# Kernel optimization log

Hardware: AMD Instinct MI355X
Metric: run time of the kernel (lower is better)

## Reference

```python
import jax, jax.numpy as jnp
import numpy as np

H = 768        # hidden_size == embedding_dim (forced by GRU input 3*H)
S = 512        # seq_len
V = 30522      # vocab_size
MAXLEN = 32    # decode steps
B = 8
NEG = -1e6


def setup_inputs() -> dict:
    key = jax.random.key(0)
    ks = jax.random.split(key, 12)
    sd = 0.02
    return {
        "encoder_outputs": jax.random.normal(ks[0], (B, S, H), jnp.float32),
        "inputs": jax.random.randint(ks[1], (B, S), 0, V),
        "cls_to": 101,
        "sep_to": 102,
        "emb": jax.random.normal(ks[2], (V, H), jnp.float32) * sd,
        "attn_w": jax.random.normal(ks[3], (H, H), jnp.float32) * sd,
        "attn_b": jnp.zeros((H,), jnp.float32),
        "copy_w": jax.random.normal(ks[4], (H, H), jnp.float32) * sd,
        "copy_b": jnp.zeros((H,), jnp.float32),
        "gru_w_ih": jax.random.normal(ks[5], (3 * H, 3 * H), jnp.float32) * sd,
        "gru_w_hh": jax.random.normal(ks[6], (3 * H, H), jnp.float32) * sd,
        "gru_b_ih": jnp.zeros((3 * H,), jnp.float32),
        "gru_b_hh": jnp.zeros((3 * H,), jnp.float32),
        "out_w": jax.random.normal(ks[7], (V, H), jnp.float32) * sd,
        "out_b": jnp.zeros((V,), jnp.float32),
    }


def _gru_cell(x, h, w_ih, w_hh, b_ih, b_hh):
    # PyTorch GRU cell, gate order (r, z, n)
    gi = x @ w_ih.T + b_ih          # [B, 3H]
    gh = h @ w_hh.T + b_hh          # [B, 3H]
    gi_r, gi_z, gi_n = jnp.split(gi, 3, axis=-1)
    gh_r, gh_z, gh_n = jnp.split(gh, 3, axis=-1)
    r = jax.nn.sigmoid(gi_r + gh_r)
    z = jax.nn.sigmoid(gi_z + gh_z)
    n = jnp.tanh(gi_n + r * gh_n)
    return (1.0 - z) * n + z * h


def reference(encoder_outputs, inputs, cls_to, sep_to, emb, attn_w, attn_b,
              copy_w, copy_b, gru_w_ih, gru_w_hh, gru_b_ih, gru_b_hh,
              out_w, out_b):
    dtype = encoder_outputs.dtype
    ext = V + S  # extended vocab (vocab + seq positions)
    one_hot = jax.nn.one_hot(inputs, ext, dtype=dtype)          # [B, S, V+S]
    missing = (one_hot.sum(axis=1) == 0).at[:, 0].set(True)     # [B, V+S]

    def step(carry, _):
        hidden, idx, sel = carry  # [B,H], [B] int, [B,H]
        # attention
        th = hidden @ attn_w.T + attn_b                          # [B,H]
        attn_scores = jnp.einsum('bsh,bh->bs', encoder_outputs, th)
        attn_weights = jax.nn.softmax(attn_scores, axis=-1)
        context = jnp.einsum('bs,bsh->bh', attn_weights, encoder_outputs)
        # embed previous token (OOV -> UNK id 3; note original uses strict >)
        idx_c = jnp.where(idx > V, 3, idx)
        embedded = emb[idx_c]                                    # [B,H]
        # GRU step
        x = jnp.concatenate([context, sel, embedded], axis=-1)   # [B,3H]
        h = _gru_cell(x, hidden, gru_w_ih, gru_w_hh, gru_b_ih, gru_b_hh)
        # copy scores
        th2 = h @ copy_w.T + copy_b
        copy_score_seq = jnp.einsum('bsh,bh->bs', encoder_outputs, th2)  # [B,S]
        copy_scores = jnp.einsum('bs,bsv->bv', copy_score_seq, one_hot)  # [B,V+S]
        copy_scores = jnp.where(missing, NEG, copy_scores)
        # generation scores
        gen = (h @ out_w.T + out_b).at[:, 0].set(NEG)            # [B,V]
        combined = jnp.concatenate([gen, copy_scores], axis=-1)  # [B,2V+S]
        probs = jax.nn.softmax(combined, axis=-1)
        gen_probs = jnp.concatenate(
            [probs[:, :V], jnp.zeros((B, S), dtype)], axis=-1)   # [B,V+S]
        final_probs = gen_probs + probs[:, V:]
        log_probs = jnp.log(final_probs + 1e-10)                 # [B,V+S]
        sampled = jnp.argmax(log_probs, axis=-1)                 # [B]
        # selective read for next step
        pos = jnp.take_along_axis(one_hot, sampled[:, None, None], axis=2)[..., 0]  # [B,S]
        sel_scores = pos * copy_score_seq
        denom = jnp.maximum(jnp.sum(jnp.abs(sel_scores), axis=1, keepdims=True), 1e-12)
        sel_new = jnp.einsum('bs,bsh->bh', sel_scores / denom, encoder_outputs)
        return (h, sampled, sel_new), (log_probs, sampled)

    init = (jnp.zeros((B, H), dtype),
            jnp.ones((B,), jnp.int32),
            jnp.zeros((B, H), dtype))
    _, (logps, samples) = jax.lax.scan(step, init, None, length=MAXLEN - 1)

    sos = jnp.zeros((B, ext), dtype).at[:, 0].set(cls_to)
    decoder_outputs = jnp.concatenate(
        [sos[:, None, :], jnp.swapaxes(logps, 0, 1)], axis=1)    # [B,MAXLEN,V+S]
    sampled_idxs = jnp.concatenate(
        [jnp.ones((B, 1), samples.dtype), samples.T], axis=1)    # [B,MAXLEN]
    return decoder_outputs, sampled_idxs
```

## Files before the change

kernel.cpp:

```cpp
#include <hip/hip_runtime.h>
#include <hip/hip_bf16.h>
#include <math.h>

#define HDIM 768
#define SDIM 512
#define VDIM 30522
#define BDIM 8
#define TLEN 32
#define H3   2304
#define VT   31034
#define NEGV -1.0e6f
#define OFF2 ((size_t)BDIM * TLEN * VT)
#define SSLICE 64
#define VSLICE 3816
#define NROWS (HDIM + VDIM + HDIM + H3)

__global__ __launch_bounds__(256) void boot_kernel(
    float* __restrict__ dout, const int* __restrict__ cls,
    float* __restrict__ hA, float* __restrict__ x,
    const float* __restrict__ emb, float* __restrict__ thb,
    float* __restrict__ ghb, const float* __restrict__ attn_b,
    const float* __restrict__ b_hh)
{
    int gidx = blockIdx.x * 256 + threadIdx.x;
    int stride = gridDim.x * 256;
    float clsv = (float)cls[0];
    for (int i = gidx; i < BDIM * VT; i += stride) {
        int b = i / VT, v = i % VT;
        dout[(size_t)b * TLEN * VT + v] = (v == 0) ? clsv : 0.f;
    }
    if (gidx < BDIM) dout[OFF2 + (size_t)gidx * TLEN] = 1.0f;
    for (int i = gidx; i < BDIM * HDIM; i += stride) {
        int b = i / HDIM, j = i % HDIM;
        hA[i] = 0.f;
        x[b * H3 + HDIM + j] = 0.f;
        x[b * H3 + 2 * HDIM + j] = emb[HDIM + j];
        thb[i] = attn_b[j];
    }
    for (int i = gidx; i < BDIM * H3; i += stride)
        ghb[i] = b_hh[i % H3];
}

__global__ __launch_bounds__(512) void grufull_kernel(
    const float* __restrict__ w_ih, const float* __restrict__ b_ih,
    const float* __restrict__ x, const float* __restrict__ ghb,
    const float* __restrict__ hin, float* __restrict__ hout)
{
    int wid = threadIdx.x >> 6, lane = threadIdx.x & 63;
    int j = blockIdx.x * 8 + wid;
    if (j >= HDIM) return;

    const float4* wr = (const float4*)(w_ih + (size_t)j * H3);
    const float4* wz = (const float4*)(w_ih + (size_t)(HDIM + j) * H3);
    const float4* wn = (const float4*)(w_ih + (size_t)(2 * HDIM + j) * H3);

    float ar[8], az[8], an[8];
#pragma unroll
    for (int b = 0; b < 8; b++) { ar[b] = 0.f; az[b] = 0.f; an[b] = 0.f; }

    for (int k4 = lane; k4 < H3 / 4; k4 += 64) {
        float4 w4r = wr[k4], w4z = wz[k4], w4n = wn[k4];
#pragma unroll
        for (int b = 0; b < 8; b++) {
            float4 x4 = ((const float4*)(x + b * H3))[k4];
            ar[b] += w4r.x * x4.x + w4r.y * x4.y + w4r.z * x4.z + w4r.w * x4.w;
            az[b] += w4z.x * x4.x + w4z.y * x4.y + w4z.z * x4.z + w4z.w * x4.w;
            an[b] += w4n.x * x4.x + w4n.y * x4.y + w4n.z * x4.z + w4n.w * x4.w;
        }
    }
#pragma unroll
    for (int b = 0; b < 8; b++) {
        float vr = ar[b], vz = az[b], vn = an[b];
        for (int off = 32; off; off >>= 1) {
            vr += __shfl_down(vr, off, 64);
            vz += __shfl_down(vz, off, 64);
            vn += __shfl_down(vn, off, 64);
        }
        ar[b] = vr; az[b] = vz; an[b] = vn;
    }
    if (lane == 0) {
        float bi_r = b_ih[j], bi_z = b_ih[HDIM + j], bi_n = b_ih[2 * HDIM + j];
#pragma unroll
        for (int b = 0; b < 8; b++) {
            float gir = ar[b] + bi_r;
            float giz = az[b] + bi_z;
            float gin = an[b] + bi_n;
            float ghr = ghb[b * H3 + j];
            float ghz = ghb[b * H3 + HDIM + j];
            float ghn = ghb[b * H3 + 2 * HDIM + j];
            float r = 1.f / (1.f + expf(-(gir + ghr)));
            float z = 1.f / (1.f + expf(-(giz + ghz)));
            float n = tanhf(gin + r * ghn);
            hout[b * HDIM + j] = (1.f - z) * n + z * hin[b * HDIM + j];
        }
    }
}

struct RowT { const float* w; const float* bias; float* dst; int stride; int neg; };

__device__ __forceinline__ RowT row_info(
    int r,
    const float* copy_w, const float* copy_b,
    const float* out_w,  const float* out_b,
    const float* attn_w, const float* attn_b,
    const float* w_hh,   const float* b_hh,
    float* th2, float* gen, float* thb, float* ghb)
{
    RowT t;
    if (r < HDIM) {
        t.w = copy_w + (size_t)r * HDIM; t.bias = copy_b + r;
        t.dst = th2 + r; t.stride = HDIM; t.neg = 0;
    } else if (r < HDIM + VDIM) {
        int v = r - HDIM;
        t.w = out_w + (size_t)v * HDIM; t.bias = out_b + v;
        t.dst = gen + v; t.stride = VDIM; t.neg = (v == 0);
    } else if (r < 2 * HDIM + VDIM) {
        int rr = r - HDIM - VDIM;
        t.w = attn_w + (size_t)rr * HDIM; t.bias = attn_b + rr;
        t.dst = thb + rr; t.stride = HDIM; t.neg = 0;
    } else {
        int rr = r - 2 * HDIM - VDIM;
        t.w = w_hh + (size_t)rr * HDIM; t.bias = b_hh + rr;
        t.dst = ghb + rr; t.stride = H3; t.neg = 0;
    }
    return t;
}

__global__ __launch_bounds__(256) void bigmv_kernel(
    const float* __restrict__ copy_w, const float* __restrict__ copy_b,
    const float* __restrict__ out_w,  const float* __restrict__ out_b,
    const float* __restrict__ attn_w, const float* __restrict__ attn_b,
    const float* __restrict__ w_hh,   const float* __restrict__ b_hh,
    const float* __restrict__ hp, float* __restrict__ th2,
    float* __restrict__ gen, float* __restrict__ thb,
    float* __restrict__ ghb)
{
    __shared__ float xs[BDIM * HDIM];
    {
        const float4* s4 = (const float4*)hp;
        float4* d4 = (float4*)xs;
#pragma unroll
        for (int i = 0; i < 6; i++)
            d4[threadIdx.x + i * 256] = s4[threadIdx.x + i * 256];
    }
    __syncthreads();

    int wid = threadIdx.x >> 6, lane = threadIdx.x & 63;
    int r0 = blockIdx.x * 16 + wid * 4;
    if (r0 >= NROWS) return;

    int rc1 = min(r0 + 1, NROWS - 1);
    int rc2 = min(r0 + 2, NROWS - 1), rc3 = min(r0 + 3, NROWS - 1);
    RowT t0 = row_info(r0,  copy_w, copy_b, out_w, out_b, attn_w, attn_b,
                       w_hh, b_hh, th2, gen, thb, ghb);
    RowT t1 = row_info(rc1, copy_w, copy_b, out_w, out_b, attn_w, attn_b,
                       w_hh, b_hh, th2, gen, thb, ghb);
    RowT t2 = row_info(rc2, copy_w, copy_b, out_w, out_b, attn_w, attn_b,
                       w_hh, b_hh, th2, gen, thb, ghb);
    RowT t3 = row_info(rc3, copy_w, copy_b, out_w, out_b, attn_w, attn_b,
                       w_hh, b_hh, th2, gen, thb, ghb);

    float a0[8], a1[8], a2[8], a3[8];
#pragma unroll
    for (int b = 0; b < 8; b++) { a0[b] = 0.f; a1[b] = 0.f; a2[b] = 0.f; a3[b] = 0.f; }

    const float4* w0 = (const float4*)t0.w;
    const float4* w1 = (const float4*)t1.w;
    const float4* w2 = (const float4*)t2.w;
    const float4* w3 = (const float4*)t3.w;

#pragma unroll
    for (int i = 0; i < 3; i++) {
        int k4 = lane + i * 64;
        float4 q0 = w0[k4], q1 = w1[k4], q2 = w2[k4], q3 = w3[k4];
#pragma unroll
        for (int b = 0; b < 8; b++) {
            float4 x4 = ((const float4*)(xs + b * HDIM))[k4];
            a0[b] += q0.x * x4.x + q0.y * x4.y + q0.z * x4.z + q0.w * x4.w;
            a1[b] += q1.x * x4.x + q1.y * x4.y + q1.z * x4.z + q1.w * x4.w;
            a2[b] += q2.x * x4.x + q2.y * x4.y + q2.z * x4.z + q2.w * x4.w;
            a3[b] += q3.x * x4.x + q3.y * x4.y + q3.z * x4.z + q3.w * x4.w;
        }
    }
#pragma unroll
    for (int b = 0; b < 8; b++) {
        float v0 = a0[b], v1 = a1[b], v2 = a2[b], v3 = a3[b];
        for (int off = 32; off; off >>= 1) {
            v0 += __shfl_down(v0, off, 64);
            v1 += __shfl_down(v1, off, 64);
            v2 += __shfl_down(v2, off, 64);
            v3 += __shfl_down(v3, off, 64);
        }
        a0[b] = v0; a1[b] = v1; a2[b] = v2; a3[b] = v3;
    }
    if (lane == 0) {
        float bb0 = t0.bias[0], bb1 = t1.bias[0], bb2 = t2.bias[0], bb3 = t3.bias[0];
#pragma unroll
        for (int b = 0; b < 8; b++) {
            t0.dst[(size_t)b * t0.stride] = t0.neg ? NEGV : a0[b] + bb0;
            if (r0 + 1 < NROWS) t1.dst[(size_t)b * t1.stride] = t1.neg ? NEGV : a1[b] + bb1;
            if (r0 + 2 < NROWS) t2.dst[(size_t)b * t2.stride] = t2.neg ? NEGV : a2[b] + bb2;
            if (r0 + 3 < NROWS) t3.dst[(size_t)b * t3.stride] = t3.neg ? NEGV : a3[b] + bb3;
        }
    }
}

__global__ __launch_bounds__(512) void combo_kernel(
    const float* __restrict__ enc, const float* __restrict__ thb,
    const float* __restrict__ th2, float* __restrict__ css,
    float* __restrict__ atC, float* __restrict__ atM, float* __restrict__ atZ,
    const float* __restrict__ gen, float* __restrict__ gM,
    float* __restrict__ gZ, int do_cg)
{
    __shared__ float sth[HDIM];
    __shared__ float sth2[HDIM];
    __shared__ float swe[SSLICE];
    __shared__ float red[8];
    int blk = blockIdx.x, b = blk >> 3, sub = blk & 7;
    int tid = threadIdx.x, wid = tid >> 6, lane = tid & 63;
    int slo = sub * SSLICE;

    for (int i = tid; i < HDIM; i += 512) {
        sth[i]  = thb[b * HDIM + i];
        sth2[i] = th2[b * HDIM + i];
    }
    __syncthreads();

    for (int j = 0; j < 8; j++) {
        int sl = wid * 8 + j, s = slo + sl;
        const float4* er = (const float4*)(enc + ((size_t)b * SDIM + s) * HDIM);
        float a1 = 0.f, a2 = 0.f;
#pragma unroll
        for (int i = 0; i < 3; i++) {
            float4 e = er[lane + i * 64];
            float4 t1 = ((const float4*)sth)[lane + i * 64];
            float4 t2 = ((const float4*)sth2)[lane + i * 64];
            a1 += e.x * t1.x + e.y * t1.y + e.z * t1.z + e.w * t1.w;
            a2 += e.x * t2.x + e.y * t2.y + e.z * t2.z + e.w * t2.w;
        }
        for (int off = 32; off; off >>= 1) {
            a1 += __shfl_down(a1, off, 64);
            a2 += __shfl_down(a2, off, 64);
        }
        if (lane == 0) {
            swe[sl] = a1;
            if (do_cg) css[b * SDIM + s] = a2;
        }
    }
    __syncthreads();

    if (tid < 64) {
        float v = swe[tid];
        float m = v;
        for (int off = 32; off; off >>= 1) m = fmaxf(m, __shfl_xor(m, off, 64));
        float e = expf(v - m);
        float z = e;
        for (int off = 32; off; off >>= 1) z += __shfl_xor(z, off, 64);
        swe[tid] = e;
        if (tid == 0) { atM[b * 8 + sub] = m; atZ[b * 8 + sub] = z; }
    }
    __syncthreads();

    for (int col = tid; col < HDIM; col += 512) {
        float acc = 0.f;
        const float* eb = enc + ((size_t)b * SDIM + slo) * HDIM + col;
#pragma unroll 8
        for (int s2 = 0; s2 < SSLICE; s2++) acc += swe[s2] * eb[s2 * HDIM];
        atC[((size_t)b * 8 + sub) * HDIM + col] = acc;
    }

    if (!do_cg) return;

    int vlo = sub * VSLICE, vhi = min(VDIM, vlo + VSLICE);
    const float* grow = gen + (size_t)b * VDIM;
    float m = -INFINITY;
    for (int v = vlo + tid; v < vhi; v += 512) m = fmaxf(m, grow[v]);
    for (int off = 32; off; off >>= 1) m = fmaxf(m, __shfl_xor(m, off, 64));
    if (lane == 0) red[wid] = m;
    __syncthreads();
    float M = red[0];
#pragma unroll
    for (int w = 1; w < 8; w++) M = fmaxf(M, red[w]);
    float z = 0.f;
    for (int v = vlo + tid; v < vhi; v += 512) z += expf(grow[v] - M);
    for (int off = 32; off; off >>= 1) z += __shfl_xor(z, off, 64);
    __syncthreads();
    if (lane == 0) red[wid] = z;
    __syncthreads();
    if (tid == 0) {
        float Z = 0.f;
#pragma unroll
        for (int w = 0; w < 8; w++) Z += red[w];
        gM[b * 8 + sub] = M;
        gZ[b * 8 + sub] = Z;
    }
}

__global__ __launch_bounds__(1024) void tailc_kernel(
    const float* __restrict__ gen, const float* __restrict__ css,
    const int* __restrict__ inputs, const float* __restrict__ genM,
    const float* __restrict__ genZ, float* __restrict__ dout,
    float* __restrict__ argV, int* __restrict__ argI, int t)
{
    __shared__ int   toks[SDIM];
    __shared__ float csss[SDIM];
    __shared__ float aggv[SDIM];
    __shared__ unsigned char ffl[SDIM];
    __shared__ float redf[1024];
    __shared__ int   redi[1024];
    int blk = blockIdx.x, b = blk >> 3, sub = blk & 7;
    int tid = threadIdx.x;

    if (tid < SDIM) {
        toks[tid] = inputs[b * SDIM + tid];
        csss[tid] = css[b * SDIM + tid];
    }
    __syncthreads();

    if (tid < SDIM) {
        int tok = toks[tid]; int isf = 0; float agg = -INFINITY;
        if (tok != 0) {
            isf = 1;
            for (int s2 = 0; s2 < tid; s2++)
                if (toks[s2] == tok) { isf = 0; break; }
            if (isf) {
                float ss = 0.f;
                for (int s2 = tid; s2 < SDIM; s2++)
                    if (toks[s2] == tok) ss += csss[s2];
                agg = ss;
            }
        }
        ffl[tid] = (unsigned char)isf;
        aggv[tid] = agg;
    }
    __syncthreads();

    redf[tid] = (tid < SDIM && ffl[tid]) ? aggv[tid] : -INFINITY;
    __syncthreads();
    for (int off = 512; off; off >>= 1) {
        if (tid < off) redf[tid] = fmaxf(redf[tid], redf[tid + off]);
        __syncthreads();
    }
    float m9 = redf[0]; __syncthreads();
    redf[tid] = (tid < SDIM && ffl[tid] && m9 > -INFINITY)
                    ? expf(aggv[tid] - m9) : 0.f;
    __syncthreads();
    for (int off = 512; off; off >>= 1) {
        if (tid < off) redf[tid] += redf[tid + off];
        __syncthreads();
    }
    float z9 = redf[0]; __syncthreads();

    float M = genM[b * 8 + 0];
#pragma unroll
    for (int i = 1; i < 8; i++) M = fmaxf(M, genM[b * 8 + i]);
    if (m9 > -INFINITY) M = fmaxf(M, m9);
    float Z = 0.f;
#pragma unroll
    for (int i = 0; i < 8; i++) Z += genZ[b * 8 + i] * expf(genM[b * 8 + i] - M);
    if (m9 > -INFINITY) Z += z9 * expf(m9 - M);
    float invZ = 1.f / Z;

    const float* grow = gen + (size_t)b * VDIM;
    float* orow = dout + ((size_t)b * TLEN + t + 1) * VT;
    int vlo = sub * VSLICE, vhi = min(VDIM, vlo + VSLICE);
    float best = -INFINITY; int bidx = 2147483647;
    for (int v = vlo + tid; v < vhi; v += 1024) {
        float pg = expf(grow[v] - M) * invZ;
        float lp = logf(pg + 1e-10f);
        orow[v] = lp;
        if (lp > best) { best = lp; bidx = v; }
    }
    if (sub == 0 && tid < SDIM) orow[VDIM + tid] = logf(1e-10f);
    __syncthreads();

    if (tid < SDIM && ffl[tid]) {
        int tok = toks[tid];
        if (tok >= vlo && tok < vhi) {
            float pc = expf(aggv[tid] - M) * invZ;
            float pg = expf(grow[tok] - M) * invZ;
            float lp = logf(pg + pc + 1e-10f);
            orow[tok] = lp;
            if (lp > best || (lp == best && tok < bidx)) { best = lp; bidx = tok; }
        }
    }
    redf[tid] = best; redi[tid] = bidx; __syncthreads();
    for (int off = 512; off; off >>= 1) {
        if (tid < off) {
            float v2 = redf[tid + off]; int i2 = redi[tid + off];
            if (v2 > redf[tid] || (v2 == redf[tid] && i2 < redi[tid])) {
                redf[tid] = v2; redi[tid] = i2;
            }
        }
        __syncthreads();
    }
    if (tid == 0) { argV[b * 8 + sub] = redf[0]; argI[b * 8 + sub] = redi[0]; }
}

__global__ __launch_bounds__(1024) void mix_kernel(
    const float* __restrict__ enc, const float* __restrict__ css,
    const int* __restrict__ inputs, const float* __restrict__ argV,
    const int* __restrict__ argI, const float* __restrict__ emb,
    float* __restrict__ dout, float* __restrict__ x,
    const float* __restrict__ atC, const float* __restrict__ atM,
    const float* __restrict__ atZ, int t, int do_tail)
{
    __shared__ int   toks[SDIM];
    __shared__ float csss[SDIM];
    __shared__ float redf[1024];
    __shared__ int   mlist[SDIM];
    __shared__ float mscore[SDIM];
    __shared__ int   wcnt[16], woff[16];
    __shared__ int   mtot;
    int bid = blockIdx.x, tid = threadIdx.x;

    if (bid >= BDIM) {
        int b = bid - BDIM;
        if (tid < HDIM) {
            float m[8], z[8];
#pragma unroll
            for (int i = 0; i < 8; i++) { m[i] = atM[b * 8 + i]; z[i] = atZ[b * 8 + i]; }
            float M = m[0];
#pragma unroll
            for (int i = 1; i < 8; i++) M = fmaxf(M, m[i]);
            float Z = 0.f;
#pragma unroll
            for (int i = 0; i < 8; i++) Z += z[i] * expf(m[i] - M);
            float acc = 0.f;
#pragma unroll
            for (int i = 0; i < 8; i++)
                acc += atC[((size_t)b * 8 + i) * HDIM + tid] * expf(m[i] - M);
            x[b * H3 + tid] = acc / Z;
        }
        return;
    }
    if (!do_tail) return;

    int b = bid;
    float best = argV[b * 8 + 0]; int samp = argI[b * 8 + 0];
#pragma unroll
    for (int i = 1; i < 8; i++) {
        float v = argV[b * 8 + i];
        if (v > best) { best = v; samp = argI[b * 8 + i]; }
    }
    if (tid == 0) dout[OFF2 + (size_t)b * TLEN + t + 1] = (float)samp;

    if (tid < SDIM) {
        toks[tid] = inputs[b * SDIM + tid];
        csss[tid] = css[b * SDIM + tid];
    }
    __syncthreads();

    int flag = (tid < SDIM) ? (toks[tid] == samp) : 0;
    redf[tid] = flag ? fabsf(csss[tid]) : 0.f;
    __syncthreads();
    for (int off = 512; off; off >>= 1) {
        if (tid < off) redf[tid] += redf[tid + off];
        __syncthreads();
    }
    float den = fmaxf(redf[0], 1e-12f);
    __syncthreads();

    unsigned long long mk = __ballot(flag);
    int wv = tid >> 6, ln = tid & 63;
    if (ln == 0) wcnt[wv] = __popcll(mk);
    __syncthreads();
    if (tid == 0) {
        int o = 0;
        for (int w = 0; w < 16; w++) { woff[w] = o; o += wcnt[w]; }
        mtot = o;
    }
    __syncthreads();
    if (flag) {
        int pos = woff[wv] + __popcll(mk & ((1ULL << ln) - 1ULL));
        mlist[pos] = tid;
        mscore[pos] = csss[tid] / den;
    }
    __syncthreads();
    int mc = mtot;

    if (tid < HDIM) {
        float sel = 0.f;
        for (int mI = 0; mI < mc; mI++)
            sel += mscore[mI] * enc[((size_t)b * SDIM + mlist[mI]) * HDIM + tid];
        x[b * H3 + HDIM + tid] = sel;
        int ic = (samp > VDIM) ? 3 : samp;
        if (ic >= VDIM) ic = VDIM - 1;
        x[b * H3 + 2 * HDIM + tid] = emb[(size_t)ic * HDIM + tid];
    }
}

extern "C" void kernel_launch(void* const* d_in, const int* in_sizes, int n_in,
                              void* d_out, int out_size, void* d_ws, size_t ws_size,
                              hipStream_t stream)
{
    const float* enc    = (const float*)d_in[0];
    const int*   inputs = (const int*)d_in[1];
    const int*   cls    = (const int*)d_in[2];
    const float* emb    = (const float*)d_in[4];
    const float* attn_w = (const float*)d_in[5];
    const float* attn_b = (const float*)d_in[6];
    const float* copy_w = (const float*)d_in[7];
    const float* copy_b = (const float*)d_in[8];
    const float* w_ih   = (const float*)d_in[9];
    const float* w_hh   = (const float*)d_in[10];
    const float* b_ih   = (const float*)d_in[11];
    const float* b_hh   = (const float*)d_in[12];
    const float* out_w  = (const float*)d_in[13];
    const float* out_b  = (const float*)d_in[14];
    float* dout = (float*)d_out;

    float* ws   = (float*)d_ws;
    float* hA   = ws;
    float* hB   = hA  + BDIM * HDIM;
    float* x    = hB  + BDIM * HDIM;
    float* thb  = x   + BDIM * H3;
    float* ghb  = thb + BDIM * HDIM;
    float* th2  = ghb + BDIM * H3;
    float* gen  = th2 + BDIM * HDIM;
    float* css  = gen + (size_t)BDIM * VDIM;
    float* atC  = css + BDIM * SDIM;
    float* atM  = atC + BDIM * 8 * HDIM;
    float* atZ  = atM + 64;
    float* gM   = atZ + 64;
    float* gZ   = gM  + 64;
    float* argV = gZ  + 64;
    int*   argI = (int*)(argV + 64);

    boot_kernel<<<512, 256, 0, stream>>>(dout, cls, hA, x, emb, thb, ghb,
                                         attn_b, b_hh);
    combo_kernel<<<64, 512, 0, stream>>>(enc, thb, th2, css, atC, atM, atZ,
                                         gen, gM, gZ, 0);
    mix_kernel<<<16, 1024, 0, stream>>>(enc, css, inputs, argV, argI, emb,
                                        dout, x, atC, atM, atZ, 0, 0);

    for (int t = 0; t < TLEN - 1; t++) {
        const float* hin  = (t & 1) ? hB : hA;
        float*       hout = (t & 1) ? hA : hB;
        grufull_kernel<<<96, 512, 0, stream>>>(w_ih, b_ih, x, ghb, hin, hout);
        bigmv_kernel<<<(NROWS + 15) / 16, 256, 0, stream>>>(
            copy_w, copy_b, out_w, out_b, attn_w, attn_b, w_hh, b_hh,
            hout, th2, gen, thb, ghb);
        combo_kernel<<<64, 512, 0, stream>>>(enc, thb, th2, css, atC, atM, atZ,
                                             gen, gM, gZ, 1);
        tailc_kernel<<<64, 1024, 0, stream>>>(gen, css, inputs, gM, gZ,
                                              dout, argV, argI, t);
        mix_kernel<<<16, 1024, 0, stream>>>(enc, css, inputs, argV, argI, emb,
                                            dout, x, atC, atM, atZ, t, 1);
    }
}
```

Measured before the change: 3.342 ms.

## Split attention and vocab slices finer and use one-wave GRU blocks

The combo kernel's sequence and vocab split goes from 8 to 32 sub-slices per batch row, so it launches 256 blocks instead of 64. The mix and tail kernels now merge 32 partial softmax results instead of 8. The GRU kernel moves to one 64-thread block per hidden unit for more independent blocks. The bigmv kernel drops its shared-memory staging of the hidden state and reads it straight from global memory, relying on cache. The aim is better GPU occupancy on the latency-bound per-step kernels, at the cost of more partial-merge work and more repeated global reads of the hidden state.

New measurement: 3.298 ms. About the same (-1.3%).

```diff
diff --git a/kernel.cpp b/kernel.cpp
--- a/kernel.cpp
+++ b/kernel.cpp
@@ -11,7 +11,9 @@
 #define VT   31034
 #define NEGV -1.0e6f
 #define OFF2 ((size_t)BDIM * TLEN * VT)
-#define SSLICE 64
+#define NSUB 32
+#define SSL  16
+#define VSL  954
 #define VSLICE 3816
 #define NROWS (HDIM + VDIM + HDIM + H3)
 
@@ -41,14 +43,13 @@
         ghb[i] = b_hh[i % H3];
 }
 
-__global__ __launch_bounds__(512) void grufull_kernel(
+__global__ __launch_bounds__(64) void grufull_kernel(
     const float* __restrict__ w_ih, const float* __restrict__ b_ih,
     const float* __restrict__ x, const float* __restrict__ ghb,
     const float* __restrict__ hin, float* __restrict__ hout)
 {
-    int wid = threadIdx.x >> 6, lane = threadIdx.x & 63;
-    int j = blockIdx.x * 8 + wid;
-    if (j >= HDIM) return;
+    int lane = threadIdx.x;
+    int j = blockIdx.x;
 
     const float4* wr = (const float4*)(w_ih + (size_t)j * H3);
     const float4* wz = (const float4*)(w_ih + (size_t)(HDIM + j) * H3);
@@ -135,16 +136,6 @@
     float* __restrict__ gen, float* __restrict__ thb,
     float* __restrict__ ghb)
 {
-    __shared__ float xs[BDIM * HDIM];
-    {
-        const float4* s4 = (const float4*)hp;
-        float4* d4 = (float4*)xs;
-#pragma unroll
-        for (int i = 0; i < 6; i++)
-            d4[threadIdx.x + i * 256] = s4[threadIdx.x + i * 256];
-    }
-    __syncthreads();
-
     int wid = threadIdx.x >> 6, lane = threadIdx.x & 63;
     int r0 = blockIdx.x * 16 + wid * 4;
     if (r0 >= NROWS) return;
@@ -168,6 +159,7 @@
     const float4* w1 = (const float4*)t1.w;
     const float4* w2 = (const float4*)t2.w;
     const float4* w3 = (const float4*)t3.w;
+    const float4* xb = (const float4*)hp;
 
 #pragma unroll
     for (int i = 0; i < 3; i++) {
@@ -175,7 +167,7 @@
         float4 q0 = w0[k4], q1 = w1[k4], q2 = w2[k4], q3 = w3[k4];
 #pragma unroll
         for (int b = 0; b < 8; b++) {
-            float4 x4 = ((const float4*)(xs + b * HDIM))[k4];
+            float4 x4 = xb[b * 192 + k4];
             a0[b] += q0.x * x4.x + q0.y * x4.y + q0.z * x4.z + q0.w * x4.w;
             a1[b] += q1.x * x4.x + q1.y * x4.y + q1.z * x4.z + q1.w * x4.w;
             a2[b] += q2.x * x4.x + q2.y * x4.y + q2.z * x4.z + q2.w * x4.w;
@@ -214,11 +206,11 @@
 {
     __shared__ float sth[HDIM];
     __shared__ float sth2[HDIM];
-    __shared__ float swe[SSLICE];
+    __shared__ float swe[SSL];
     __shared__ float red[8];
-    int blk = blockIdx.x, b = blk >> 3, sub = blk & 7;
+    int blk = blockIdx.x, b = blk >> 5, sub = blk & 31;
     int tid = threadIdx.x, wid = tid >> 6, lane = tid & 63;
-    int slo = sub * SSLICE;
+    int slo = sub * SSL;
 
     for (int i = tid; i < HDIM; i += 512) {
         sth[i]  = thb[b * HDIM + i];
@@ -226,8 +218,8 @@
     }
     __syncthreads();
 
-    for (int j = 0; j < 8; j++) {
-        int sl = wid * 8 + j, s = slo + sl;
+    for (int j = 0; j < 2; j++) {
+        int sl = wid * 2 + j, s = slo + sl;
         const float4* er = (const float4*)(enc + ((size_t)b * SDIM + s) * HDIM);
         float a1 = 0.f, a2 = 0.f;
 #pragma unroll
@@ -249,29 +241,27 @@
     }
     __syncthreads();
 
-    if (tid < 64) {
-        float v = swe[tid];
-        float m = v;
-        for (int off = 32; off; off >>= 1) m = fmaxf(m, __shfl_xor(m, off, 64));
-        float e = expf(v - m);
-        float z = e;
-        for (int off = 32; off; off >>= 1) z += __shfl_xor(z, off, 64);
-        swe[tid] = e;
-        if (tid == 0) { atM[b * 8 + sub] = m; atZ[b * 8 + sub] = z; }
+    if (tid == 0) {
+        float m = swe[0];
+        for (int i = 1; i < SSL; i++) m = fmaxf(m, swe[i]);
+        float z = 0.f;
+        for (int i = 0; i < SSL; i++) { float e = expf(swe[i] - m); swe[i] = e; z += e; }
+        atM[b * NSUB + sub] = m;
+        atZ[b * NSUB + sub] = z;
     }
     __syncthreads();
 
     for (int col = tid; col < HDIM; col += 512) {
         float acc = 0.f;
         const float* eb = enc + ((size_t)b * SDIM + slo) * HDIM + col;
-#pragma unroll 8
-        for (int s2 = 0; s2 < SSLICE; s2++) acc += swe[s2] * eb[s2 * HDIM];
-        atC[((size_t)b * 8 + sub) * HDIM + col] = acc;
+#pragma unroll
+        for (int s2 = 0; s2 < SSL; s2++) acc += swe[s2] * eb[s2 * HDIM];
+        atC[((size_t)b * NSUB + sub) * HDIM + col] = acc;
     }
 
     if (!do_cg) return;
 
-    int vlo = sub * VSLICE, vhi = min(VDIM, vlo + VSLICE);
+    int vlo = sub * VSL, vhi = min(VDIM, vlo + VSL);
     const float* grow = gen + (size_t)b * VDIM;
     float m = -INFINITY;
     for (int v = vlo + tid; v < vhi; v += 512) m = fmaxf(m, grow[v]);
@@ -291,8 +281,8 @@
         float Z = 0.f;
 #pragma unroll
         for (int w = 0; w < 8; w++) Z += red[w];
-        gM[b * 8 + sub] = M;
-        gZ[b * 8 + sub] = Z;
+        gM[b * NSUB + sub] = M;
+        gZ[b * NSUB + sub] = Z;
     }
 }
 
@@ -351,13 +341,14 @@
     }
     float z9 = redf[0]; __syncthreads();
 
-    float M = genM[b * 8 + 0];
-#pragma unroll
-    for (int i = 1; i < 8; i++) M = fmaxf(M, genM[b * 8 + i]);
+    float M = genM[b * NSUB + 0];
+#pragma unroll
+    for (int i = 1; i < NSUB; i++) M = fmaxf(M, genM[b * NSUB + i]);
     if (m9 > -INFINITY) M = fmaxf(M, m9);
     float Z = 0.f;
 #pragma unroll
-    for (int i = 0; i < 8; i++) Z += genZ[b * 8 + i] * expf(genM[b * 8 + i] - M);
+    for (int i = 0; i < NSUB; i++)
+        Z += genZ[b * NSUB + i] * expf(genM[b * NSUB + i] - M);
     if (m9 > -INFINITY) Z += z9 * expf(m9 - M);
     float invZ = 1.f / Z;
 
@@ -417,19 +408,16 @@
     if (bid >= BDIM) {
         int b = bid - BDIM;
         if (tid < HDIM) {
-            float m[8], z[8];
-#pragma unroll
-            for (int i = 0; i < 8; i++) { m[i] = atM[b * 8 + i]; z[i] = atZ[b * 8 + i]; }
-            float M = m[0];
-#pragma unroll
-            for (int i = 1; i < 8; i++) M = fmaxf(M, m[i]);
-            float Z = 0.f;
-#pragma unroll
-            for (int i = 0; i < 8; i++) Z += z[i] * expf(m[i] - M);
-            float acc = 0.f;
-#pragma unroll
-            for (int i = 0; i < 8; i++)
-                acc += atC[((size_t)b * 8 + i) * HDIM + tid] * expf(m[i] - M);
+            float M = atM[b * NSUB];
+#pragma unroll
+            for (int i = 1; i < NSUB; i++) M = fmaxf(M, atM[b * NSUB + i]);
+            float Z = 0.f, acc = 0.f;
+#pragma unroll
+            for (int i = 0; i < NSUB; i++) {
+                float sc = expf(atM[b * NSUB + i] - M);
+                Z += atZ[b * NSUB + i] * sc;
+                acc += atC[((size_t)b * NSUB + i) * HDIM + tid] * sc;
+            }
             x[b * H3 + tid] = acc / Z;
         }
         return;
@@ -520,29 +508,29 @@
     float* gen  = th2 + BDIM * HDIM;
     float* css  = gen + (size_t)BDIM * VDIM;
     float* atC  = css + BDIM * SDIM;
-    float* atM  = atC + BDIM * 8 * HDIM;
-    float* atZ  = atM + 64;
-    float* gM   = atZ + 64;
-    float* gZ   = gM  + 64;
-    float* argV = gZ  + 64;
+    float* atM  = atC + (size_t)BDIM * NSUB * HDIM;
+    float* atZ  = atM + BDIM * NSUB;
+    float* gM   = atZ + BDIM * NSUB;
+    float* gZ   = gM  + BDIM * NSUB;
+    float* argV = gZ  + BDIM * NSUB;
     int*   argI = (int*)(argV + 64);
 
     boot_kernel<<<512, 256, 0, stream>>>(dout, cls, hA, x, emb, thb, ghb,
                                          attn_b, b_hh);
-    combo_kernel<<<64, 512, 0, stream>>>(enc, thb, th2, css, atC, atM, atZ,
-                                         gen, gM, gZ, 0);
+    combo_kernel<<<256, 512, 0, stream>>>(enc, thb, th2, css, atC, atM, atZ,
+                                          gen, gM, gZ, 0);
     mix_kernel<<<16, 1024, 0, stream>>>(enc, css, inputs, argV, argI, emb,
                                         dout, x, atC, atM, atZ, 0, 0);
 
     for (int t = 0; t < TLEN - 1; t++) {
         const float* hin  = (t & 1) ? hB : hA;
         float*       hout = (t & 1) ? hA : hB;
-        grufull_kernel<<<96, 512, 0, stream>>>(w_ih, b_ih, x, ghb, hin, hout);
+        grufull_kernel<<<HDIM, 64, 0, stream>>>(w_ih, b_ih, x, ghb, hin, hout);
         bigmv_kernel<<<(NROWS + 15) / 16, 256, 0, stream>>>(
             copy_w, copy_b, out_w, out_b, attn_w, attn_b, w_hh, b_hh,
             hout, th2, gen, thb, ghb);
-        combo_kernel<<<64, 512, 0, stream>>>(enc, thb, th2, css, atC, atM, atZ,
-                                             gen, gM, gZ, 1);
+        combo_kernel<<<256, 512, 0, stream>>>(enc, thb, th2, css, atC, atM, atZ,
+                                              gen, gM, gZ, 1);
         tailc_kernel<<<64, 1024, 0, stream>>>(gen, css, inputs, gM, gZ,
                                               dout, argV, argI, t);
         mix_kernel<<<16, 1024, 0, stream>>>(enc, css, inputs, argV, argI, emb,
```
